# Optimization experiments

Measured on AMD Instinct MI355X. Metric: run time of the kernel, lower is better.

The kernel has to match this reference:

```python
import jax, jax.numpy as jnp
import numpy as np

IN_FEATURES = 4096
OUT_FEATURES = 768
N_BITS = 8
BATCH = 4096


def setup_inputs() -> dict:
    key = jax.random.key(0)
    k1, k2, k3 = jax.random.split(key, 3)
    latent = jax.random.uniform(k1, (BATCH, IN_FEATURES), dtype=jnp.float32)
    true_sum = jax.random.uniform(k2, (BATCH, OUT_FEATURES * N_BITS), dtype=jnp.float32)
    # kaiming-normal-ish init: std = sqrt(2 / fan_in)
    weight = jax.random.normal(k3, (IN_FEATURES, OUT_FEATURES * N_BITS), dtype=jnp.float32) * np.sqrt(2.0 / IN_FEATURES)
    return {"latent": latent, "true_sum": true_sum, "weight": weight, "n_bits": N_BITS}


def reference(latent, true_sum, weight, n_bits):
    in_features = weight.shape[0]
    batch = latent.shape[0]
    # powers of two, MSB negated (two's-complement style decode)
    powers = (2.0 ** jnp.arange(n_bits, dtype=jnp.float32))
    powers = powers.at[-1].multiply(-1.0)

    prob_weights = jax.nn.sigmoid(weight)                      # [in, out*n_bits]
    # decode soft bits -> integer-valued weights: [in, out]
    int_weights = (prob_weights.reshape(in_features, -1, n_bits) * powers).sum(-1)
    # decode target bits -> integer-valued sums: [batch, out]
    int_sum = (true_sum.reshape(batch, -1, n_bits) * powers).sum(-1)

    # (latent.unsqueeze(-1) * int_weights).sum(-2) is exactly a GEMM
    pred = latent @ int_weights                                # [batch, out]

    scale_factor = 2.0 ** (n_bits - 1)
    recon_loss = jnp.mean((pred - int_sum) ** 2) / scale_factor
    polarize_loss = jnp.mean(prob_weights * (1.0 - prob_weights))
    return (recon_loss, polarize_loss)
```

## Files before the change

### kernel.cpp

```cpp
#include <hip/hip_runtime.h>
#include <stdint.h>

#define IN_F   4096
#define OUT_F  768
#define NB     8
#define BATCH  4096
#define WCOLS  (OUT_F*NB)
#define PREDN  (BATCH*OUT_F)

typedef short  bf16x8  __attribute__((ext_vector_type(8)));
typedef float  f32x4   __attribute__((ext_vector_type(4)));
typedef unsigned short ushort8 __attribute__((ext_vector_type(8)));

__device__ __forceinline__ unsigned short f2bf(float f){
    union { float f; uint32_t u; } v; v.f = f;
    uint32_t u = v.u;
    u += 0x7FFFu + ((u >> 16) & 1u);
    return (unsigned short)(u >> 16);
}

__device__ __forceinline__ void gload16(const void* g, void* l){
    __builtin_amdgcn_global_load_lds(
        (const __attribute__((address_space(1))) unsigned int*)g,
        (__attribute__((address_space(3))) unsigned int*)l, 16, 0, 0);
}

__launch_bounds__(256)
__global__ void decode_all(const float* __restrict__ w,
                           const float* __restrict__ lat,
                           unsigned short* __restrict__ bt,
                           unsigned short* __restrict__ abf,
                           float* __restrict__ polp){
    __shared__ unsigned short tile[64][70];
    __shared__ float part[4];
    const int tid = threadIdx.x;
    const int bid = blockIdx.x;
    if (bid < 768){
        const int k0 = (bid & 63) * 64;
        const int n0 = (bid >> 6) * 64;
        const int j     = tid & 63;
        const int ibase = (tid >> 6) * 16;
        float pol = 0.f;
        #pragma unroll 4
        for (int r = 0; r < 16; ++r){
            int i = ibase + r;
            const float4* src = (const float4*)(w + (size_t)(k0+i)*WCOLS + (size_t)(n0+j)*8);
            float4 a = src[0], b = src[1];
            float x[8] = {a.x,a.y,a.z,a.w,b.x,b.y,b.z,b.w};
            float p[8];
            #pragma unroll
            for (int q = 0; q < 8; ++q){
                p[q] = 1.f / (1.f + __expf(-x[q]));
                pol += p[q] * (1.f - p[q]);
            }
            float iw = p[0] + 2.f*p[1] + 4.f*p[2] + 8.f*p[3]
                     + 16.f*p[4] + 32.f*p[5] + 64.f*p[6] - 128.f*p[7];
            tile[j][i] = f2bf(iw);
        }
        #pragma unroll
        for (int off = 32; off; off >>= 1) pol += __shfl_down(pol, off);
        if ((tid & 63) == 0) part[tid >> 6] = pol;
        __syncthreads();
        const int nrow = tid >> 4;
        const int kb   = (tid & 15) * 4;
        #pragma unroll
        for (int q = 0; q < 4; ++q){
            int n = nrow + q*16;
            uint2 v;
            v.x = *(const unsigned int*)&tile[n][kb];
            v.y = *(const unsigned int*)&tile[n][kb+2];
            *(uint2*)(bt + (size_t)(n0+n)*IN_F + k0 + kb) = v;
        }
        if (tid == 0) polp[bid] = part[0]+part[1]+part[2]+part[3];
    } else {
        int idx = ((bid - 768) * 256 + tid) * 8;
        const float4* p = (const float4*)(lat + idx);
        float4 a = p[0], b = p[1];
        ushort8 o;
        o[0]=f2bf(a.x); o[1]=f2bf(a.y); o[2]=f2bf(a.z); o[3]=f2bf(a.w);
        o[4]=f2bf(b.x); o[5]=f2bf(b.y); o[6]=f2bf(b.z); o[7]=f2bf(b.w);
        *(ushort8*)(abf + idx) = o;
    }
}

#define BM 128
#define BN 96
#define BK 64
#define NTH 32
#define ABYTES (BM*BK*2)
#define BBYTES (BN*BK*2)
#define BUFB   (ABYTES+BBYTES)

__launch_bounds__(256)
__global__ void gemm_pred(const unsigned short* __restrict__ abf,
                          const unsigned short* __restrict__ bt,
                          float* __restrict__ pred){
    __shared__ __align__(16) char smem[2*BUFB];
    const int tid = threadIdx.x;
    const int w   = tid >> 6;
    const int l   = tid & 63;
    const int s   = l & 15, g = l >> 4;
    const int wr  = w >> 1, wc = w & 1;
    const int bid  = blockIdx.x;
    const int half = bid >> 8;
    const int rem  = bid & 255;
    const int m0   = (rem >> 3) * BM;
    const int n0   = (rem & 7)  * BN;
    const int kb   = half * (NTH*BK);

    f32x4 accv[4][3];
    #pragma unroll
    for (int m = 0; m < 4; ++m)
        #pragma unroll
        for (int n = 0; n < 3; ++n)
            accv[m][n] = (f32x4){0.f,0.f,0.f,0.f};

    const int c8  = tid & 7;
    const int r0  = tid >> 3;
    const int scw = ((c8 ^ (r0 & 7)) << 3);
    const unsigned short* aS = abf + (size_t)(m0 + r0) * IN_F + kb + scw;
    const unsigned short* bS = bt  + (size_t)(n0 + r0) * IN_F + kb + scw;

    #define STAGE(kt, base) do {                                           \
        const int _ko = (kt) * BK;                                         \
        char* _ad = (base) + tid*16;                                       \
        char* _bd = (base) + ABYTES + tid*16;                              \
        _Pragma("unroll")                                                  \
        for (int _i = 0; _i < 4; ++_i)                                     \
            gload16(aS + (size_t)_i*32*IN_F + _ko, _ad + _i*4096);         \
        _Pragma("unroll")                                                  \
        for (int _i = 0; _i < 3; ++_i)                                     \
            gload16(bS + (size_t)_i*32*IN_F + _ko, _bd + _i*4096);         \
    } while (0)

    #define COMPUTE(base) do {                                             \
        char* _Ab = (base);                                                \
        char* _Bb = (base) + ABYTES;                                       \
        _Pragma("unroll")                                                  \
        for (int _kk = 0; _kk < 2; ++_kk){                                 \
            bf16x8 _af[4], _bf[3];                                         \
            _Pragma("unroll")                                              \
            for (int _m = 0; _m < 4; ++_m){                                \
                int _r  = wr*64 + _m*16 + s;                               \
                int _ch = _r*8 + ((_kk*4 + g) ^ (_r & 7));                 \
                _af[_m] = *(const bf16x8*)(_Ab + _ch*16);                  \
            }                                                              \
            _Pragma("unroll")                                              \
            for (int _n = 0; _n < 3; ++_n){                                \
                int _r  = wc*48 + _n*16 + s;                               \
                int _ch = _r*8 + ((_kk*4 + g) ^ (_r & 7));                 \
                _bf[_n] = *(const bf16x8*)(_Bb + _ch*16);                  \
            }                                                              \
            __builtin_amdgcn_s_setprio(1);                                 \
            _Pragma("unroll")                                              \
            for (int _m = 0; _m < 4; ++_m)                                 \
                _Pragma("unroll")                                          \
                for (int _n = 0; _n < 3; ++_n)                             \
                    accv[_m][_n] = __builtin_amdgcn_mfma_f32_16x16x32_bf16(\
                        _af[_m], _bf[_n], accv[_m][_n], 0, 0, 0);          \
            __builtin_amdgcn_s_setprio(0);                                 \
        }                                                                  \
    } while (0)

    char* b0 = smem;
    char* b1 = smem + BUFB;
    STAGE(0, b0);
    __syncthreads();
    for (int t = 0; t < NTH; ++t){
        if (t + 1 < NTH) STAGE(t + 1, (t & 1) ? b0 : b1);
        COMPUTE((t & 1) ? b1 : b0);
        __syncthreads();
    }

    float* slab = pred + (size_t)half * PREDN;
    #pragma unroll
    for (int m = 0; m < 4; ++m){
        int rbase = m0 + wr*64 + m*16 + g*4;
        #pragma unroll
        for (int n = 0; n < 3; ++n){
            int col = n0 + wc*48 + n*16 + s;
            #pragma unroll
            for (int jj = 0; jj < 4; ++jj)
                slab[(size_t)(rbase+jj)*OUT_F + col] = accv[m][n][jj];
        }
    }
}

__launch_bounds__(256)
__global__ void loss_pass(const float* __restrict__ pred,
                          const float* __restrict__ ts,
                          float* __restrict__ lossp){
    __shared__ float part[4];
    const int tid = threadIdx.x;
    const int e0  = (blockIdx.x * 256 + tid) * 2;
    float local = 0.f;
    #pragma unroll
    for (int q = 0; q < 2; ++q){
        int e = e0 + q;
        float p = pred[e] + pred[(size_t)PREDN + e];
        const float4* r = (const float4*)(ts + (size_t)e * 8);
        float4 x = r[0], y = r[1];
        float is = x.x + 2.f*x.y + 4.f*x.z + 8.f*x.w
                 + 16.f*y.x + 32.f*y.y + 64.f*y.z - 128.f*y.w;
        float d = p - is;
        local += d*d;
    }
    #pragma unroll
    for (int off = 32; off; off >>= 1) local += __shfl_down(local, off);
    if ((tid & 63) == 0) part[tid >> 6] = local;
    __syncthreads();
    if (tid == 0) lossp[blockIdx.x] = part[0]+part[1]+part[2]+part[3];
}

__launch_bounds__(256)
__global__ void finalize(const float* __restrict__ lossp,
                         const float* __restrict__ polp,
                         float* __restrict__ out){
    __shared__ float sm[2][4];
    const int tid = threadIdx.x;
    float a = 0.f, b = 0.f;
    for (int i = tid; i < 6144; i += 256) a += lossp[i];
    for (int i = tid; i < 768;  i += 256) b += polp[i];
    #pragma unroll
    for (int off = 32; off; off >>= 1){
        a += __shfl_down(a, off);
        b += __shfl_down(b, off);
    }
    if ((tid & 63) == 0){ sm[0][tid >> 6] = a; sm[1][tid >> 6] = b; }
    __syncthreads();
    if (tid == 0){
        float sa = sm[0][0]+sm[0][1]+sm[0][2]+sm[0][3];
        float sb = sm[1][0]+sm[1][1]+sm[1][2]+sm[1][3];
        out[0] = sa * (1.0f / ((float)BATCH * (float)OUT_F * 128.0f));
        out[1] = sb * (1.0f / ((float)IN_F * (float)WCOLS));
    }
}

extern "C" void kernel_launch(void* const* d_in, const int* in_sizes, int n_in,
                              void* d_out, int out_size, void* d_ws, size_t ws_size,
                              hipStream_t stream){
    const float* latent   = (const float*)d_in[0];
    const float* true_sum = (const float*)d_in[1];
    const float* weight   = (const float*)d_in[2];
    char* ws = (char*)d_ws;
    float* lossp = (float*)ws;
    float* polp  = (float*)(ws + 32768);
    unsigned short* bt  = (unsigned short*)(ws + 65536);
    unsigned short* abf = (unsigned short*)(ws + 65536 + 6291456);
    float* pred = (float*)(ws + 65536 + 6291456 + 33554432);
    float* out = (float*)d_out;

    decode_all<<<768 + 8192, 256, 0, stream>>>(weight, latent, bt, abf, polp);
    gemm_pred<<<512, 256, 0, stream>>>(abf, bt, pred);
    loss_pass<<<PREDN/512, 256, 0, stream>>>(pred, true_sum, lossp);
    finalize<<<1, 256, 0, stream>>>(lossp, polp, out);
}
```

Measured before the change: 109.8 us.

## Split decode into smaller-tile weight decode and separate latent cast kernel

Replaces the combined decode kernel with a 32x32-tile weight decode that issues all eight vector loads up front, then computes the sigmoid with a fast reciprocal and writes the transposed tile with 16-byte stores. A separate latent cast kernel handles four float4 loads per thread. The loss pass is restructured to batch its loads before the arithmetic. The aim is more memory-level parallelism and better occupancy in these bandwidth-bound stages. The cost is an extra kernel launch, four times as many polarize partials to reduce, and a slightly less exact reciprocal.

```diff
diff --git a/kernel.cpp b/kernel.cpp
--- a/kernel.cpp
+++ b/kernel.cpp
@@ -10,7 +10,8 @@
 
 typedef short  bf16x8  __attribute__((ext_vector_type(8)));
 typedef float  f32x4   __attribute__((ext_vector_type(4)));
-typedef unsigned short ushort8 __attribute__((ext_vector_type(8)));
+typedef float  f32x2   __attribute__((ext_vector_type(2)));
+typedef unsigned short ushort4v __attribute__((ext_vector_type(4)));
 
 __device__ __forceinline__ unsigned short f2bf(float f){
     union { float f; uint32_t u; } v; v.f = f;
@@ -25,61 +26,85 @@
         (__attribute__((address_space(3))) unsigned int*)l, 16, 0, 0);
 }
 
-__launch_bounds__(256)
-__global__ void decode_all(const float* __restrict__ w,
-                           const float* __restrict__ lat,
-                           unsigned short* __restrict__ bt,
-                           unsigned short* __restrict__ abf,
-                           float* __restrict__ polp){
-    __shared__ unsigned short tile[64][70];
+#define SBAR() __builtin_amdgcn_sched_barrier(0)
+
+__device__ __forceinline__ float sig8dot(const f32x4 a, const f32x4 b, float& pol){
+    float s0 = __builtin_amdgcn_rcpf(1.f + __expf(-a[0]));
+    float s1 = __builtin_amdgcn_rcpf(1.f + __expf(-a[1]));
+    float s2 = __builtin_amdgcn_rcpf(1.f + __expf(-a[2]));
+    float s3 = __builtin_amdgcn_rcpf(1.f + __expf(-a[3]));
+    float s4 = __builtin_amdgcn_rcpf(1.f + __expf(-b[0]));
+    float s5 = __builtin_amdgcn_rcpf(1.f + __expf(-b[1]));
+    float s6 = __builtin_amdgcn_rcpf(1.f + __expf(-b[2]));
+    float s7 = __builtin_amdgcn_rcpf(1.f + __expf(-b[3]));
+    pol += s0*(1.f-s0) + s1*(1.f-s1) + s2*(1.f-s2) + s3*(1.f-s3)
+         + s4*(1.f-s4) + s5*(1.f-s5) + s6*(1.f-s6) + s7*(1.f-s7);
+    return s0 + 2.f*s1 + 4.f*s2 + 8.f*s3
+         + 16.f*s4 + 32.f*s5 + 64.f*s6 - 128.f*s7;
+}
+
+__launch_bounds__(256)
+__global__ void decode_weight(const float* __restrict__ w,
+                              unsigned short* __restrict__ bt,
+                              float* __restrict__ polp){
+    __shared__ unsigned short tile[32][34];
     __shared__ float part[4];
     const int tid = threadIdx.x;
-    const int bid = blockIdx.x;
-    if (bid < 768){
-        const int k0 = (bid & 63) * 64;
-        const int n0 = (bid >> 6) * 64;
-        const int j     = tid & 63;
-        const int ibase = (tid >> 6) * 16;
-        float pol = 0.f;
-        #pragma unroll 4
-        for (int r = 0; r < 16; ++r){
-            int i = ibase + r;
-            const float4* src = (const float4*)(w + (size_t)(k0+i)*WCOLS + (size_t)(n0+j)*8);
-            float4 a = src[0], b = src[1];
-            float x[8] = {a.x,a.y,a.z,a.w,b.x,b.y,b.z,b.w};
-            float p[8];
-            #pragma unroll
-            for (int q = 0; q < 8; ++q){
-                p[q] = 1.f / (1.f + __expf(-x[q]));
-                pol += p[q] * (1.f - p[q]);
-            }
-            float iw = p[0] + 2.f*p[1] + 4.f*p[2] + 8.f*p[3]
-                     + 16.f*p[4] + 32.f*p[5] + 64.f*p[6] - 128.f*p[7];
-            tile[j][i] = f2bf(iw);
-        }
-        #pragma unroll
-        for (int off = 32; off; off >>= 1) pol += __shfl_down(pol, off);
-        if ((tid & 63) == 0) part[tid >> 6] = pol;
-        __syncthreads();
-        const int nrow = tid >> 4;
-        const int kb   = (tid & 15) * 4;
-        #pragma unroll
-        for (int q = 0; q < 4; ++q){
-            int n = nrow + q*16;
-            uint2 v;
-            v.x = *(const unsigned int*)&tile[n][kb];
-            v.y = *(const unsigned int*)&tile[n][kb+2];
-            *(uint2*)(bt + (size_t)(n0+n)*IN_F + k0 + kb) = v;
-        }
-        if (tid == 0) polp[bid] = part[0]+part[1]+part[2]+part[3];
-    } else {
-        int idx = ((bid - 768) * 256 + tid) * 8;
-        const float4* p = (const float4*)(lat + idx);
-        float4 a = p[0], b = p[1];
-        ushort8 o;
-        o[0]=f2bf(a.x); o[1]=f2bf(a.y); o[2]=f2bf(a.z); o[3]=f2bf(a.w);
-        o[4]=f2bf(b.x); o[5]=f2bf(b.y); o[6]=f2bf(b.z); o[7]=f2bf(b.w);
-        *(ushort8*)(abf + idx) = o;
+    const int k0 = blockIdx.x * 32;
+    const int n0 = blockIdx.y * 32;
+    const int kl = (tid >> 4) * 2;
+    const int nq = (tid & 15) * 2;
+    const f32x4* wf4 = (const f32x4*)w;
+
+    f32x4 r0a, r0b, r0c, r0d, r1a, r1b, r1c, r1d;
+    {
+        size_t b0 = (size_t)(k0 + kl)     * 1536 + (size_t)(n0 + nq) * 2;
+        size_t b1 = (size_t)(k0 + kl + 1) * 1536 + (size_t)(n0 + nq) * 2;
+        r0a = wf4[b0];   r0b = wf4[b0+1]; r0c = wf4[b0+2]; r0d = wf4[b0+3];
+        r1a = wf4[b1];   r1b = wf4[b1+1]; r1c = wf4[b1+2]; r1d = wf4[b1+3];
+    }
+    SBAR();
+    float pol = 0.f;
+    tile[nq  ][kl  ] = f2bf(sig8dot(r0a, r0b, pol));
+    tile[nq+1][kl  ] = f2bf(sig8dot(r0c, r0d, pol));
+    tile[nq  ][kl+1] = f2bf(sig8dot(r1a, r1b, pol));
+    tile[nq+1][kl+1] = f2bf(sig8dot(r1c, r1d, pol));
+
+    #pragma unroll
+    for (int off = 32; off; off >>= 1) pol += __shfl_down(pol, off);
+    if ((tid & 63) == 0) part[tid >> 6] = pol;
+    __syncthreads();
+    if (tid < 128){
+        const int n  = tid >> 2;
+        const int dw = tid & 3;
+        uint4 v;
+        v.x = *(const unsigned int*)&tile[n][dw*8];
+        v.y = *(const unsigned int*)&tile[n][dw*8+2];
+        v.z = *(const unsigned int*)&tile[n][dw*8+4];
+        v.w = *(const unsigned int*)&tile[n][dw*8+6];
+        *(uint4*)(bt + (size_t)(n0+n)*IN_F + k0 + dw*8) = v;
+    }
+    if (tid == 0)
+        polp[blockIdx.y * 128 + blockIdx.x] = part[0]+part[1]+part[2]+part[3];
+}
+
+__launch_bounds__(256)
+__global__ void latent_cast(const float* __restrict__ lat,
+                            unsigned short* __restrict__ abf){
+    const int tid  = threadIdx.x;
+    const int base = blockIdx.x * 4096;
+    const f32x4* p = (const f32x4*)(lat + base);
+    ushort4v* o = (ushort4v*)(abf + base);
+    f32x4 v[4];
+    #pragma unroll
+    for (int i = 0; i < 4; ++i) v[i] = p[tid + i*256];
+    SBAR();
+    #pragma unroll
+    for (int i = 0; i < 4; ++i){
+        ushort4v u;
+        u[0]=f2bf(v[i][0]); u[1]=f2bf(v[i][1]);
+        u[2]=f2bf(v[i][2]); u[3]=f2bf(v[i][3]);
+        o[tid + i*256] = u;
     }
 }
 
@@ -193,18 +218,18 @@
     __shared__ float part[4];
     const int tid = threadIdx.x;
     const int e0  = (blockIdx.x * 256 + tid) * 2;
-    float local = 0.f;
-    #pragma unroll
-    for (int q = 0; q < 2; ++q){
-        int e = e0 + q;
-        float p = pred[e] + pred[(size_t)PREDN + e];
-        const float4* r = (const float4*)(ts + (size_t)e * 8);
-        float4 x = r[0], y = r[1];
-        float is = x.x + 2.f*x.y + 4.f*x.z + 8.f*x.w
-                 + 16.f*y.x + 32.f*y.y + 64.f*y.z - 128.f*y.w;
-        float d = p - is;
-        local += d*d;
-    }
+    const f32x4* tsp = (const f32x4*)(ts + (size_t)e0 * 8);
+    f32x4 t0 = tsp[0], t1 = tsp[1], t2 = tsp[2], t3 = tsp[3];
+    f32x2 p0 = *(const f32x2*)(pred + e0);
+    f32x2 p1 = *(const f32x2*)(pred + (size_t)PREDN + e0);
+    SBAR();
+    float is0 = t0[0] + 2.f*t0[1] + 4.f*t0[2] + 8.f*t0[3]
+              + 16.f*t1[0] + 32.f*t1[1] + 64.f*t1[2] - 128.f*t1[3];
+    float is1 = t2[0] + 2.f*t2[1] + 4.f*t2[2] + 8.f*t2[3]
+              + 16.f*t3[0] + 32.f*t3[1] + 64.f*t3[2] - 128.f*t3[3];
+    float d0 = (p0[0] + p1[0]) - is0;
+    float d1 = (p0[1] + p1[1]) - is1;
+    float local = d0*d0 + d1*d1;
     #pragma unroll
     for (int off = 32; off; off >>= 1) local += __shfl_down(local, off);
     if ((tid & 63) == 0) part[tid >> 6] = local;
@@ -220,7 +245,7 @@
     const int tid = threadIdx.x;
     float a = 0.f, b = 0.f;
     for (int i = tid; i < 6144; i += 256) a += lossp[i];
-    for (int i = tid; i < 768;  i += 256) b += polp[i];
+    for (int i = tid; i < 3072; i += 256) b += polp[i];
     #pragma unroll
     for (int off = 32; off; off >>= 1){
         a += __shfl_down(a, off);
@@ -250,7 +275,8 @@
     float* pred = (float*)(ws + 65536 + 6291456 + 33554432);
     float* out = (float*)d_out;
 
-    decode_all<<<768 + 8192, 256, 0, stream>>>(weight, latent, bt, abf, polp);
+    decode_weight<<<dim3(IN_F/32, OUT_F/32), 256, 0, stream>>>(weight, bt, polp);
+    latent_cast<<<(BATCH*IN_F)/4096, 256, 0, stream>>>(latent, abf);
     gemm_pred<<<512, 256, 0, stream>>>(abf, bt, pred);
     loss_pass<<<PREDN/512, 256, 0, stream>>>(pred, true_sum, lossp);
     finalize<<<1, 256, 0, stream>>>(lossp, polp, out);
```

Result: slower. 114.6 us (+4.4%).
